# Performance work log

Hardware: AMD Instinct MI355X
Metric: run time of the kernel (lower is better)

The kernel has to match this reference:

```python
import jax, jax.numpy as jnp
import numpy as np

HID = 768
NH = 12
HD = HID // NH
EPS = 1e-12


def _layernorm(x, g, b):
    m = x.mean(-1, keepdims=True)
    v = ((x - m) ** 2).mean(-1, keepdims=True)
    return (x - m) / jnp.sqrt(v + EPS) * g + b


def _mha_block(x, mask, Wq, bq, Wk, bk, Wv, bv, Wo, bo, ln_g, ln_b):
    # x: [B,S,H]; mask broadcastable to [B,NH,S,S] (additive)
    B, S, _ = x.shape
    split = lambda t: t.reshape(B, S, NH, HD).transpose(0, 2, 1, 3)  # [B,NH,S,HD]
    q = split(x @ Wq + bq)
    k = split(x @ Wk + bk)
    v = split(x @ Wv + bv)
    scores = jnp.einsum('bhqd,bhkd->bhqk', q, k) / np.float32(np.sqrt(HD)) + mask
    probs = jax.nn.softmax(scores, axis=-1)
    ctx = jnp.einsum('bhqk,bhkd->bhqd', probs, v)
    ctx = ctx.transpose(0, 2, 1, 3).reshape(B, S, HID)
    # BertSelfOutput: dense + residual + LayerNorm
    return _layernorm(ctx @ Wo + bo + x, ln_g, ln_b)


def setup_inputs() -> dict:
    key = jax.random.key(0)
    ks = jax.random.split(key, 32)
    B, S = 32, 512
    scale = 0.02
    W = lambda i, di, do: jax.random.normal(ks[i], (di, do), jnp.float32) * scale
    inp = {
        'hidden_states': jax.random.normal(ks[0], (B, S, HID), jnp.float32),
        'attention_mask': jnp.zeros((B, 1, 1, S), jnp.float32),
        # token-level attention params
        'Wq': W(1, HID, HID), 'bq': jnp.zeros((HID,), jnp.float32),
        'Wk': W(2, HID, HID), 'bk': jnp.zeros((HID,), jnp.float32),
        'Wv': W(3, HID, HID), 'bv': jnp.zeros((HID,), jnp.float32),
        'Wao': W(4, HID, HID), 'bao': jnp.zeros((HID,), jnp.float32),
        'ln1_g': jnp.ones((HID,), jnp.float32), 'ln1_b': jnp.zeros((HID,), jnp.float32),
        # dialog (CLS-level) attention params
        'dWq': W(5, HID, HID), 'dbq': jnp.zeros((HID,), jnp.float32),
        'dWk': W(6, HID, HID), 'dbk': jnp.zeros((HID,), jnp.float32),
        'dWv': W(7, HID, HID), 'dbv': jnp.zeros((HID,), jnp.float32),
        'dWo': W(8, HID, HID), 'dbo': jnp.zeros((HID,), jnp.float32),
        'dln_g': jnp.ones((HID,), jnp.float32), 'dln_b': jnp.zeros((HID,), jnp.float32),
        # FFN params
        'Wi': W(9, HID, 4 * HID), 'bi': jnp.zeros((4 * HID,), jnp.float32),
        'Wo2': W(10, 4 * HID, HID), 'bo2': jnp.zeros((HID,), jnp.float32),
        'ln2_g': jnp.ones((HID,), jnp.float32), 'ln2_b': jnp.zeros((HID,), jnp.float32),
        'turns': 8,
    }
    return inp


def reference(hidden_states, attention_mask,
              Wq, bq, Wk, bk, Wv, bv, Wao, bao, ln1_g, ln1_b,
              dWq, dbq, dWk, dbk, dWv, dbv, dWo, dbo, dln_g, dln_b,
              Wi, bi, Wo2, bo2, ln2_g, ln2_b, turns):
    # 1) token-level self-attention + SelfOutput
    x = _mha_block(hidden_states, attention_mask,
                   Wq, bq, Wk, bk, Wv, bv, Wao, bao, ln1_g, ln1_b)
    # 2) hierarchical dialog attention over per-turn CLS tokens
    bs = x.shape[0] // turns
    cls = x[:, 0].reshape(bs, turns, HID)
    pos = jnp.arange(turns)
    # faithful to source: (j >= i) -> -10000 (masks diagonal and future)
    cmask = (pos[None, :] >= pos[:, None]).astype(x.dtype) * (-10000.0)
    cmask = cmask[None, None, :, :]  # broadcast to [bs, NH, turns, turns]
    cls = _mha_block(cls, cmask, dWq, dbq, dWk, dbk, dWv, dbv, dWo, dbo, dln_g, dln_b)
    x = x.at[:, 0].set(cls.reshape(-1, HID))
    # 3) FFN: intermediate (gelu) + output dense + residual + LayerNorm
    inter = jax.nn.gelu(x @ Wi + bi, approximate=False)
    out = _layernorm(inter @ Wo2 + bo2 + x, ln2_g, ln2_b)
    return out
```

## Files before the change

### kernel.cpp

```cpp
#include <hip/hip_runtime.h>
#include <hip/hip_bf16.h>
#include <math.h>

using bf16 = __hip_bfloat16;
typedef __attribute__((ext_vector_type(8))) __bf16 bf16x8;
typedef __attribute__((ext_vector_type(4))) float f32x4;

__device__ __forceinline__ float b2f(bf16 x){ return __bfloat162float(x); }
__device__ __forceinline__ bf16  f2b(float x){ return __float2bfloat16(x); }
__device__ __forceinline__ float ldf(const float* p, size_t i){ return p[i]; }
__device__ __forceinline__ float ldf(const bf16*  p, size_t i){ return b2f(p[i]); }
__device__ __forceinline__ void stf(float* p, size_t i, float v){ p[i] = v; }
__device__ __forceinline__ void stf(bf16*  p, size_t i, float v){ p[i] = f2b(v); }

__device__ __forceinline__ float gelu_f(float v){
  float u = v*(0.7978845608f + 0.0356774081f*v*v);
  float e = __expf(2.f*u);
  float t = 1.f - 2.f/(e+1.f);
  return 0.5f*v*(1.f+t);
}

typedef const __attribute__((address_space(1))) unsigned int* gas_u32p;
typedef __attribute__((address_space(3))) unsigned int* las_u32p;
__device__ __forceinline__ void gl_lds16(const bf16* g, bf16* l){
  __builtin_amdgcn_global_load_lds((gas_u32p)(const void*)g, (las_u32p)(void*)l, 16, 0, 0);
}

#define MFMA16 __builtin_amdgcn_mfma_f32_16x16x32_bf16

#define LGKM(N) do { \
  asm volatile("s_waitcnt lgkmcnt(" #N ")" ::: "memory"); \
  __builtin_amdgcn_sched_barrier(0); \
} while(0)

#define NHEAD 12
#define HDIM  64
#define HID   768
#define SEQ   512
#define BATCH 32
#define ROWS  (BATCH*SEQ)
#define QKVW  2304
#define QCH   128
#define NCHUNK (SEQ/QCH)
#define FT    128

template<int EPI, typename TR>
__global__ __launch_bounds__(512,2)
void gemm8p(const bf16* __restrict__ A, int lda,
            const bf16* __restrict__ Bt, int ldb,
            bf16* __restrict__ C, int ldc, int K,
            const float* __restrict__ bias,
            const TR* __restrict__ res, int ldres)
{
  __shared__ __align__(16) bf16 tileLds[4][256*64];

  const int tid  = threadIdx.x;
  const int wave = tid>>6, lane = tid&63;
  const int r = lane&15, qd = lane>>4;
  const int wr = wave>>2, wc = wave&3;
  const int m0 = blockIdx.y*256, n0 = blockIdx.x*256;
  const int NTK = K>>6;
  const int wbase = wave*512;

  const int sr = tid>>3, sp = tid&7;
  const bf16* pA = A  + (size_t)(m0+sr)*lda + ((sp^(sr&7))<<3);
  const bf16* pB = Bt + (size_t)(n0+sr)*ldb + ((sp^(sr&7))<<3);

  auto stage = [&](int H){
    const int u = H>>2, idx = H&3, bufi = u&1;
    const size_t kof = (size_t)u*64;
    if (idx==0){
      gl_lds16(pA + kof,                    tileLds[bufi*2] + wbase);
      gl_lds16(pA + kof + (size_t)64*lda,   tileLds[bufi*2] + wbase + 4096);
    } else if (idx==3){
      gl_lds16(pA + kof + (size_t)128*lda,  tileLds[bufi*2] + 8192 + wbase);
      gl_lds16(pA + kof + (size_t)192*lda,  tileLds[bufi*2] + 8192 + wbase + 4096);
    } else {
      const int h = idx-1;
      gl_lds16(pB + kof + (size_t)(h*128)*ldb,
               tileLds[bufi*2+1] + h*8192 + wbase);
      gl_lds16(pB + kof + (size_t)(h*128+64)*ldb,
               tileLds[bufi*2+1] + h*8192 + wbase + 4096);
    }
  };

  auto rdA = [&](const bf16* base, int mi, int ks)->bf16x8{
    const int row = mi*32 + wr*16 + r;
    return *(const bf16x8*)(base + row*64 + ((((ks<<2)|qd) ^ (r&7))<<3));
  };
  auto rdB = [&](const bf16* base, int nj, int ks)->bf16x8{
    const int row = nj*64 + wc*16 + r;
    return *(const bf16x8*)(base + row*64 + ((((ks<<2)|qd) ^ (r&7))<<3));
  };

  #pragma unroll
  for (int H=0; H<7; ++H) stage(H);
  asm volatile("s_waitcnt vmcnt(6)" ::: "memory");
  __builtin_amdgcn_s_barrier();

  f32x4 acc[8][4] = {};

  for (int t=0; t<NTK; ++t){
    const bf16* a = tileLds[(t&1)*2];
    const bf16* b = tileLds[(t&1)*2+1];
    const int Hb = 4*t + 6;
    const int Hmax = 4*NTK;
    bf16x8 af[4][2], bn0[2][2], bn1[2][2];

    af[0][0]=rdA(a,0,0); af[0][1]=rdA(a,0,1);
    af[1][0]=rdA(a,1,0); af[1][1]=rdA(a,1,1);
    bn0[0][0]=rdB(b,0,0); bn0[0][1]=rdB(b,0,1);
    bn0[1][0]=rdB(b,1,0); bn0[1][1]=rdB(b,1,1);
    __builtin_amdgcn_sched_barrier(0);
    af[2][0]=rdA(a,2,0); af[2][1]=rdA(a,2,1);
    af[3][0]=rdA(a,3,0); af[3][1]=rdA(a,3,1);
    if (Hb+1 < Hmax) stage(Hb+1);
    LGKM(4);
    __builtin_amdgcn_s_setprio(1);
    #pragma unroll
    for (int mi=0;mi<2;mi++)
      #pragma unroll
      for (int nj=0;nj<2;nj++){
        acc[mi][nj] = MFMA16(af[mi][0], bn0[nj][0], acc[mi][nj],0,0,0);
        acc[mi][nj] = MFMA16(af[mi][1], bn0[nj][1], acc[mi][nj],0,0,0);
      }
    LGKM(0);
    #pragma unroll
    for (int mi=2;mi<4;mi++)
      #pragma unroll
      for (int nj=0;nj<2;nj++){
        acc[mi][nj] = MFMA16(af[mi][0], bn0[nj][0], acc[mi][nj],0,0,0);
        acc[mi][nj] = MFMA16(af[mi][1], bn0[nj][1], acc[mi][nj],0,0,0);
      }
    __builtin_amdgcn_s_setprio(0);
    __builtin_amdgcn_s_barrier();

    bn1[0][0]=rdB(b,2,0); bn1[0][1]=rdB(b,2,1);
    __builtin_amdgcn_sched_barrier(0);
    bn1[1][0]=rdB(b,3,0); bn1[1][1]=rdB(b,3,1);
    if (Hb+2 < Hmax) stage(Hb+2);
    LGKM(2);
    __builtin_amdgcn_s_setprio(1);
    #pragma unroll
    for (int mi=0;mi<4;mi++){
      acc[mi][2] = MFMA16(af[mi][0], bn1[0][0], acc[mi][2],0,0,0);
      acc[mi][2] = MFMA16(af[mi][1], bn1[0][1], acc[mi][2],0,0,0);
    }
    LGKM(0);
    #pragma unroll
    for (int mi=0;mi<4;mi++){
      acc[mi][3] = MFMA16(af[mi][0], bn1[1][0], acc[mi][3],0,0,0);
      acc[mi][3] = MFMA16(af[mi][1], bn1[1][1], acc[mi][3],0,0,0);
    }
    __builtin_amdgcn_s_setprio(0);
    __builtin_amdgcn_s_barrier();

    af[0][0]=rdA(a,4,0); af[0][1]=rdA(a,4,1);
    af[1][0]=rdA(a,5,0); af[1][1]=rdA(a,5,1);
    __builtin_amdgcn_sched_barrier(0);
    af[2][0]=rdA(a,6,0); af[2][1]=rdA(a,6,1);
    af[3][0]=rdA(a,7,0); af[3][1]=rdA(a,7,1);
    if (Hb+3 < Hmax) stage(Hb+3);
    LGKM(4);
    __builtin_amdgcn_s_setprio(1);
    #pragma unroll
    for (int mi=0;mi<2;mi++)
      #pragma unroll
      for (int nj=0;nj<2;nj++){
        acc[4+mi][2+nj] = MFMA16(af[mi][0], bn1[nj][0], acc[4+mi][2+nj],0,0,0);
        acc[4+mi][2+nj] = MFMA16(af[mi][1], bn1[nj][1], acc[4+mi][2+nj],0,0,0);
      }
    LGKM(0);
    #pragma unroll
    for (int mi=2;mi<4;mi++)
      #pragma unroll
      for (int nj=0;nj<2;nj++){
        acc[4+mi][2+nj] = MFMA16(af[mi][0], bn1[nj][0], acc[4+mi][2+nj],0,0,0);
        acc[4+mi][2+nj] = MFMA16(af[mi][1], bn1[nj][1], acc[4+mi][2+nj],0,0,0);
      }
    __builtin_amdgcn_s_setprio(0);
    __builtin_amdgcn_s_barrier();

    if (Hb+4 < Hmax) stage(Hb+4);
    __builtin_amdgcn_s_setprio(1);
    #pragma unroll
    for (int mi=0;mi<4;mi++)
      #pragma unroll
      for (int nj=0;nj<2;nj++){
        acc[4+mi][nj] = MFMA16(af[mi][0], bn0[nj][0], acc[4+mi][nj],0,0,0);
        acc[4+mi][nj] = MFMA16(af[mi][1], bn0[nj][1], acc[4+mi][nj],0,0,0);
      }
    __builtin_amdgcn_s_setprio(0);
    if (t < NTK-2) { asm volatile("s_waitcnt vmcnt(6)" ::: "memory"); }
    else           { asm volatile("s_waitcnt vmcnt(0)" ::: "memory"); }
    __builtin_amdgcn_s_barrier();
  }

  float bs[4];
  #pragma unroll
  for (int nj=0;nj<4;nj++)
    bs[nj] = bias ? bias[n0 + nj*64 + wc*16 + r] : 0.f;
  #pragma unroll
  for (int mi=0;mi<8;mi++){
    #pragma unroll
    for (int nj=0;nj<4;nj++){
      #pragma unroll
      for (int i=0;i<4;i++){
        const int mm = m0 + mi*32 + wr*16 + qd*4 + i;
        const int nn = n0 + nj*64 + wc*16 + r;
        float v = acc[mi][nj][i] + bs[nj];
        if (EPI==1) v = gelu_f(v);
        if (EPI==2) v += ldf(res, (size_t)mm*ldres + nn);
        C[(size_t)mm*ldc + nn] = f2b(v);
      }
    }
  }
}

__global__ __launch_bounds__(256)
void flash_attn(const bf16* __restrict__ qkv, const bf16* __restrict__ vtb,
                const float* __restrict__ mask, bf16* __restrict__ ctx)
{
  const int qc = blockIdx.x;
  const int z  = blockIdx.y;
  const int b  = z / NHEAD, h = z - b*NHEAD;
  const int q0 = qc*QCH;

  __shared__ __align__(16) bf16 Qs[QCH*64];
  __shared__ __align__(16) bf16 Ks[FT*64];
  __shared__ __align__(16) bf16 Vts[64*FT];
  __shared__ float smask[FT];
  bf16* Ps = Ks;

  const int tid = threadIdx.x;
  const int wave = tid>>6, lane = tid&63;
  const int r = lane&15, qd = lane>>4;
  const int wr = wave;

  const bf16* Qg = qkv + ((size_t)(b*SEQ + q0))*QKVW + h*HDIM;
  const bf16* Kg = qkv + ((size_t)b*SEQ)*QKVW + 768 + h*HDIM;
  const bf16* Vg = vtb + (size_t)z*HDIM*SEQ;

  for (int c0=0;c0<1024;c0+=256){
    int c = c0+tid, row = c>>3, pos = c&7;
    gl_lds16(Qg + (size_t)row*QKVW + ((pos^(row&7))*8),
             Qs + (size_t)(c0 + wave*64)*8);
  }

  f32x4 accO[2][4] = {};
  float mrun[2][4], lrun[2][4];
  #pragma unroll
  for (int a=0;a<2;a++)
    #pragma unroll
    for (int i2=0;i2<4;i2++){ mrun[a][i2]=-1e30f; lrun[a][i2]=0.f; }

  for (int k0=0; k0<SEQ; k0+=FT){
    __syncthreads();
    for (int c0=0;c0<1024;c0+=256){
      int c = c0+tid, row = c>>3, pos = c&7;
      gl_lds16(Kg + (size_t)(k0+row)*QKVW + ((pos^(row&7))*8),
               Ks + (size_t)(c0 + wave*64)*8);
    }
    for (int c0=0;c0<1024;c0+=256){
      int c = c0+tid, row = c>>4, pos = c&15;
      gl_lds16(Vg + (size_t)row*SEQ + k0 + ((pos^(row&7))*8),
               Vts + (size_t)(c0 + wave*64)*8);
    }
    if (tid < FT) smask[tid] = mask[(size_t)b*SEQ + k0 + tid];
    __syncthreads();

    f32x4 accS[2][8] = {};
    #pragma unroll
    for (int ks=0; ks<2; ks++){
      bf16x8 af[2], bfv[8];
      #pragma unroll
      for (int mi=0;mi<2;mi++){
        int row = wr*32 + mi*16 + r;
        int jr = ks*4 + qd;
        af[mi] = *(const bf16x8*)(Qs + row*64 + ((jr^(row&7))*8));
      }
      #pragma unroll
      for (int ni=0;ni<8;ni++){
        int row = ni*16 + r;
        int jr = ks*4 + qd;
        bfv[ni] = *(const bf16x8*)(Ks + row*64 + ((jr^(row&7))*8));
      }
      #pragma unroll
      for (int mi=0;mi<2;mi++)
        #pragma unroll
        for (int ni=0;ni<8;ni++)
          accS[mi][ni] = MFMA16(af[mi], bfv[ni], accS[mi][ni], 0,0,0);
    }

    #pragma unroll
    for (int mi=0;mi<2;mi++){
      #pragma unroll
      for (int i=0;i<4;i++){
        float mx = -1e30f;
        #pragma unroll
        for (int ni=0;ni<8;ni++){
          float v = accS[mi][ni][i]*0.125f + smask[ni*16+r];
          accS[mi][ni][i] = v;
          mx = fmaxf(mx, v);
        }
        #pragma unroll
        for (int off=1; off<16; off<<=1) mx = fmaxf(mx, __shfl_xor(mx, off));
        float mnew = fmaxf(mrun[mi][i], mx);
        float alpha = __expf(mrun[mi][i] - mnew);
        mrun[mi][i] = mnew;
        float ssum = 0.f;
        #pragma unroll
        for (int ni=0;ni<8;ni++){
          float p = __expf(accS[mi][ni][i] - mnew);
          accS[mi][ni][i] = p;
          ssum += p;
        }
        #pragma unroll
        for (int off=1; off<16; off<<=1) ssum += __shfl_xor(ssum, off);
        lrun[mi][i] = lrun[mi][i]*alpha + ssum;
        #pragma unroll
        for (int ni=0;ni<4;ni++) accO[mi][ni][i] *= alpha;
      }
    }

    #pragma unroll
    for (int half=0; half<2; half++){
      __syncthreads();
      #pragma unroll
      for (int mi=0;mi<2;mi++){
        #pragma unroll
        for (int i=0;i<4;i++){
          int row = wr*32 + mi*16 + qd*4 + i;
          #pragma unroll
          for (int nj=0;nj<4;nj++){
            int colL = nj*16 + r;
            int chunk = colL>>3;
            Ps[row*64 + ((chunk^(row&7))*8) + (colL&7)] = f2b(accS[mi][half*4+nj][i]);
          }
        }
      }
      __syncthreads();
      #pragma unroll
      for (int ks=0; ks<2; ks++){
        bf16x8 af[2], bfv[4];
        #pragma unroll
        for (int mi=0;mi<2;mi++){
          int row = wr*32 + mi*16 + r;
          int jr = ks*4 + qd;
          af[mi] = *(const bf16x8*)(Ps + row*64 + ((jr^(row&7))*8));
        }
        #pragma unroll
        for (int ni=0;ni<4;ni++){
          int row = ni*16 + r;
          int jrv = half*8 + ks*4 + qd;
          bfv[ni] = *(const bf16x8*)(Vts + row*FT + ((jrv^(row&7))*8));
        }
        #pragma unroll
        for (int mi=0;mi<2;mi++)
          #pragma unroll
          for (int ni=0;ni<4;ni++)
            accO[mi][ni] = MFMA16(af[mi], bfv[ni], accO[mi][ni], 0,0,0);
      }
    }
  }

  bf16* Cg = ctx + ((size_t)(b*SEQ + q0))*HID + h*HDIM;
  #pragma unroll
  for (int mi=0;mi<2;mi++)
    #pragma unroll
    for (int i=0;i<4;i++){
      int row = wr*32 + mi*16 + qd*4 + i;
      float invl = 1.0f/lrun[mi][i];
      #pragma unroll
      for (int ni=0;ni<4;ni++)
        Cg[(size_t)row*HID + ni*16 + r] = f2b(accO[mi][ni][i]*invl);
    }
}

__global__ void transpose_cast(const float* __restrict__ in, bf16* __restrict__ out,
                               int R, int C)
{
  __shared__ float tile[32][33];
  int bc = blockIdx.x*32, br = blockIdx.y*32;
  int tx = threadIdx.x, ty = threadIdx.y;
  #pragma unroll
  for (int i=ty;i<32;i+=8)
    tile[i][tx] = in[(size_t)(br+i)*C + bc+tx];
  __syncthreads();
  #pragma unroll
  for (int i=ty;i<32;i+=8)
    out[(size_t)(bc+i)*R + br+tx] = f2b(tile[tx][i]);
}

__global__ void transpose_cast4(const float* __restrict__ w0, const float* __restrict__ w1,
                                const float* __restrict__ w2, const float* __restrict__ w3,
                                bf16* __restrict__ out)
{
  const float* in = blockIdx.z==0?w0 : blockIdx.z==1?w1 : blockIdx.z==2?w2 : w3;
  bf16* o = out + (size_t)blockIdx.z*768*768;
  __shared__ float tile[32][33];
  int bc = blockIdx.x*32, br = blockIdx.y*32;
  int tx = threadIdx.x, ty = threadIdx.y;
  #pragma unroll
  for (int i=ty;i<32;i+=8)
    tile[i][tx] = in[(size_t)(br+i)*768 + bc+tx];
  __syncthreads();
  #pragma unroll
  for (int i=ty;i<32;i+=8)
    o[(size_t)(bc+i)*768 + br+tx] = f2b(tile[tx][i]);
}

__global__ __launch_bounds__(256)
void castX(const float* __restrict__ in, bf16* __restrict__ out)
{
  int i = blockIdx.x*256 + threadIdx.x;
  float4 f = ((const float4*)in)[i];
  union{ unsigned long long u; __bf16 h[4]; } pk;
  pk.h[0]=(__bf16)f.x; pk.h[1]=(__bf16)f.y; pk.h[2]=(__bf16)f.z; pk.h[3]=(__bf16)f.w;
  ((unsigned long long*)out)[i] = pk.u;
}

__global__ void concat_bias(const float* __restrict__ a, const float* __restrict__ b,
                            const float* __restrict__ c, float* __restrict__ o)
{
  int i = blockIdx.x*256 + threadIdx.x;
  if (i < 768) o[i] = a[i];
  else if (i < 1536) o[i] = b[i-768];
  else if (i < 2304) o[i] = c[i-1536];
}

__global__ void vtrans(const bf16* __restrict__ v, bf16* __restrict__ vt)
{
  int z = blockIdx.z; int b = z/NHEAD, h = z - b*NHEAD;
  int d0 = blockIdx.x*32, s0 = blockIdx.y*32;
  __shared__ bf16 t[32][33];
  int tx = threadIdx.x, ty = threadIdx.y;
  #pragma unroll
  for (int i=ty;i<32;i+=8)
    t[i][tx] = v[(size_t)(b*SEQ + s0+i)*QKVW + h*HDIM + d0+tx];
  __syncthreads();
  #pragma unroll
  for (int i=ty;i<32;i+=8)
    vt[(size_t)z*HDIM*SEQ + (size_t)(d0+i)*SEQ + s0+tx] = t[tx][i];
}

template<typename TO>
__global__ __launch_bounds__(256)
void ln768(const bf16* __restrict__ y, const float* __restrict__ g,
           const float* __restrict__ be, TO* __restrict__ dst)
{
  size_t row = blockIdx.x;
  const bf16* yr = y + row*HID;
  int t = threadIdx.x;
  float x0 = b2f(yr[t]), x1 = b2f(yr[t+256]), x2 = b2f(yr[t+512]);
  float s = x0+x1+x2, q = x0*x0+x1*x1+x2*x2;
  #pragma unroll
  for (int off=32; off; off>>=1){ s += __shfl_xor(s, off); q += __shfl_xor(q, off); }
  __shared__ float rs[4], rq[4];
  int wv = t>>6;
  if ((t&63)==0){ rs[wv]=s; rq[wv]=q; }
  __syncthreads();
  s = rs[0]+rs[1]+rs[2]+rs[3];
  q = rq[0]+rq[1]+rq[2]+rq[3];
  float mean = s*(1.0f/HID);
  float var  = q*(1.0f/HID) - mean*mean;
  float inv  = rsqrtf(var + 1e-12f);
  TO* dr = dst + row*HID;
  stf(dr, t,     (x0-mean)*inv*g[t    ] + be[t    ]);
  stf(dr, t+256, (x1-mean)*inv*g[t+256] + be[t+256]);
  stf(dr, t+512, (x2-mean)*inv*g[t+512] + be[t+512]);
}

__global__ __launch_bounds__(256)
void cls_proj(const bf16* __restrict__ x2,
              const float* __restrict__ Wq, const float* __restrict__ bq,
              const float* __restrict__ Wk, const float* __restrict__ bk,
              const float* __restrict__ Wv, const float* __restrict__ bv,
              bf16* __restrict__ oq, bf16* __restrict__ ok, bf16* __restrict__ ov)
{
  int mat = blockIdx.x, row = blockIdx.y;
  const float* W  = mat==0 ? Wq : (mat==1 ? Wk : Wv);
  const float* bi = mat==0 ? bq : (mat==1 ? bk : bv);
  bf16* out       = mat==0 ? oq : (mat==1 ? ok : ov);
  __shared__ float a[HID];
  const bf16* xr = x2 + (size_t)row*SEQ*HID;
  for (int i=threadIdx.x;i<HID;i+=256) a[i] = b2f(xr[i]);
  __syncthreads();
  for (int c0=0;c0<HID;c0+=256){
    int col = c0 + threadIdx.x;
    float acc = 0.f;
    for (int k=0;k<HID;k++) acc += a[k]*W[(size_t)k*HID + col];
    out[(size_t)row*HID + col] = f2b(acc + bi[col]);
  }
}

__global__ __launch_bounds__(64)
void cls_attn(const bf16* __restrict__ q, const bf16* __restrict__ k,
              const bf16* __restrict__ v, bf16* __restrict__ ctx)
{
  int z = blockIdx.x; int bb = z/NHEAD, h = z - bb*NHEAD;
  __shared__ float P[8][8];
  int t = threadIdx.x;
  int qi = t>>3, ki = t&7;
  float s = 0.f;
  for (int d=0; d<HDIM; d++)
    s += b2f(q[(size_t)(bb*8+qi)*HID + h*HDIM + d]) *
         b2f(k[(size_t)(bb*8+ki)*HID + h*HDIM + d]);
  s = s*0.125f + (ki >= qi ? -10000.0f : 0.0f);
  float m = s;
  #pragma unroll
  for (int off=4; off; off>>=1) m = fmaxf(m, __shfl_xor(m, off, 8));
  float e = __expf(s - m);
  float sum = e;
  #pragma unroll
  for (int off=4; off; off>>=1) sum += __shfl_xor(sum, off, 8);
  P[qi][ki] = e/sum;
  __syncthreads();
  for (int q2=0; q2<8; q2++){
    float acc = 0.f;
    #pragma unroll
    for (int k2=0; k2<8; k2++)
      acc += P[q2][k2] * b2f(v[(size_t)(bb*8+k2)*HID + h*HDIM + t]);
    ctx[(size_t)(bb*8+q2)*HID + h*HDIM + t] = f2b(acc);
  }
}

__global__ __launch_bounds__(256)
void cls_out(const bf16* __restrict__ ctx, const float* __restrict__ Wo,
             const float* __restrict__ bo, const float* __restrict__ g,
             const float* __restrict__ be, bf16* __restrict__ x2)
{
  int row = blockIdx.x;
  __shared__ float a[HID];
  __shared__ float yrow[HID];
  const bf16* cr = ctx + (size_t)row*HID;
  bf16* xr = x2 + (size_t)row*SEQ*HID;
  for (int i=threadIdx.x;i<HID;i+=256) a[i] = b2f(cr[i]);
  __syncthreads();
  for (int c0=0;c0<HID;c0+=256){
    int col = c0 + threadIdx.x;
    float acc = 0.f;
    for (int k=0;k<HID;k++) acc += a[k]*Wo[(size_t)k*HID + col];
    yrow[col] = acc + bo[col] + b2f(xr[col]);
  }
  __syncthreads();
  int t = threadIdx.x;
  float x0 = yrow[t], x1 = yrow[t+256], x2v = yrow[t+512];
  float s = x0+x1+x2v, qq = x0*x0+x1*x1+x2v*x2v;
  #pragma unroll
  for (int off=32; off; off>>=1){ s += __shfl_xor(s, off); qq += __shfl_xor(qq, off); }
  __shared__ float rs[4], rq[4];
  int wv = t>>6;
  if ((t&63)==0){ rs[wv]=s; rq[wv]=qq; }
  __syncthreads();
  s = rs[0]+rs[1]+rs[2]+rs[3];
  qq = rq[0]+rq[1]+rq[2]+rq[3];
  float mean = s*(1.0f/HID);
  float var  = qq*(1.0f/HID) - mean*mean;
  float inv  = rsqrtf(var + 1e-12f);
  xr[t    ] = f2b((x0 -mean)*inv*g[t    ] + be[t    ]);
  xr[t+256] = f2b((x1 -mean)*inv*g[t+256] + be[t+256]);
  xr[t+512] = f2b((x2v-mean)*inv*g[t+512] + be[t+512]);
}

extern "C" void kernel_launch(void* const* d_in, const int* in_sizes, int n_in,
                              void* d_out, int out_size, void* d_ws, size_t ws_size,
                              hipStream_t stream)
{
  const float* X    = (const float*)d_in[0];
  const float* AM   = (const float*)d_in[1];
  const float* Wq   = (const float*)d_in[2];  const float* bq  = (const float*)d_in[3];
  const float* Wk   = (const float*)d_in[4];  const float* bk  = (const float*)d_in[5];
  const float* Wv   = (const float*)d_in[6];  const float* bv  = (const float*)d_in[7];
  const float* Wao  = (const float*)d_in[8];  const float* bao = (const float*)d_in[9];
  const float* ln1g = (const float*)d_in[10]; const float* ln1b= (const float*)d_in[11];
  const float* dWq  = (const float*)d_in[12]; const float* dbq = (const float*)d_in[13];
  const float* dWk  = (const float*)d_in[14]; const float* dbk = (const float*)d_in[15];
  const float* dWv  = (const float*)d_in[16]; const float* dbv = (const float*)d_in[17];
  const float* dWo  = (const float*)d_in[18]; const float* dbo = (const float*)d_in[19];
  const float* dlng = (const float*)d_in[20]; const float* dlnb= (const float*)d_in[21];
  const float* Wi   = (const float*)d_in[22]; const float* bi  = (const float*)d_in[23];
  const float* Wo2  = (const float*)d_in[24]; const float* bo2 = (const float*)d_in[25];
  const float* ln2g = (const float*)d_in[26]; const float* ln2b= (const float*)d_in[27];
  float* OUT = (float*)d_out;

  char* wp = (char*)d_ws;
  auto alloc = [&](size_t elems)->bf16*{
    bf16* p = (bf16*)wp;
    wp += ((elems*sizeof(bf16) + 255)/256)*256;
    return p;
  };
  bf16* wtq  = alloc(768*768);
  bf16* wtk  = alloc(768*768);
  bf16* wtv  = alloc(768*768);
  bf16* wtao = alloc(768*768);
  bf16* wti  = alloc((size_t)768*3072);
  bf16* wto2 = alloc((size_t)3072*768);
  float* bqkv = (float*)alloc(2304*2);
  bf16* qkv  = alloc((size_t)ROWS*QKVW);
  bf16* vtb  = alloc((size_t)ROWS*HID);
  bf16* inter = qkv;
  bf16* scb  = alloc((size_t)ROWS*HID);
  bf16* yb   = scb;
  bf16* x2   = scb;
  bf16* ctxb = alloc((size_t)ROWS*HID);
  bf16* xb   = ctxb;
  bf16* clsq = alloc(32*HID);
  bf16* clsk = alloc(32*HID);
  bf16* clsv = alloc(32*HID);
  bf16* clsc = alloc(32*HID);
  (void)wtk; (void)wtv;

  dim3 T32(32,8);
  transpose_cast4<<<dim3(24,24,4), T32, 0, stream>>>(Wq, Wk, Wv, Wao, wtq);
  transpose_cast<<<dim3(96,24), T32, 0, stream>>>(Wi,  wti, 768, 3072);
  transpose_cast<<<dim3(24,96), T32, 0, stream>>>(Wo2, wto2,3072, 768);
  concat_bias<<<9,256,0,stream>>>(bq, bk, bv, bqkv);
  castX<<<ROWS*HID/4/256,256,0,stream>>>(X, xb);

  gemm8p<0,float><<<dim3(9,64),512,0,stream>>>(
      xb,768,  wtq,768,  qkv,QKVW, 768, bqkv, (const float*)nullptr, 0);

  vtrans<<<dim3(2,16,BATCH*NHEAD), T32, 0, stream>>>(qkv + 1536, vtb);

  flash_attn<<<dim3(NCHUNK, BATCH*NHEAD),256,0,stream>>>(qkv, vtb, AM, ctxb);

  gemm8p<2,float><<<dim3(3,64),512,0,stream>>>(
      ctxb,768,  wtao,768,  yb,768, 768, bao, X, 768);
  ln768<bf16><<<ROWS,256,0,stream>>>(yb, ln1g, ln1b, x2);

  cls_proj<<<dim3(3,32),256,0,stream>>>(x2, dWq,dbq, dWk,dbk, dWv,dbv,
                                        clsq, clsk, clsv);
  cls_attn<<<48,64,0,stream>>>(clsq, clsk, clsv, clsc);
  cls_out<<<32,256,0,stream>>>(clsc, dWo, dbo, dlng, dlnb, x2);

  gemm8p<1,float><<<dim3(12,64),512,0,stream>>>(
      x2,768,  wti,768,  inter,3072, 768, bi, (const float*)nullptr, 0);
  gemm8p<2,bf16><<<dim3(3,64),512,0,stream>>>(
      inter,3072,  wto2,3072,  yb,768, 3072, bo2, x2, 768);
  ln768<float><<<ROWS,256,0,stream>>>(yb, ln2g, ln2b, OUT);
}
```

Before: 825.8 us.

## Prefetch next K/V tiles during compute and keep Q in registers in flash attention

Restructures the flash-attention loop so the next K tile is loaded right after the QK^T MFMAs and the next V tile right after the PV MFMAs. This overlaps global-to-LDS traffic with softmax and matmul work. Q fragments are now loaded once straight into registers, and P gets its own LDS buffer so the two per-half barriers can be dropped. The softmax switches to exp2 with pre-scaled logits and reads mask values into registers instead of through shared memory. The cost is more register pressure, and correctness now depends on each wave touching only its own P rows.

After: 829.0 us. No clear change (+0.4%).

```diff
diff --git a/kernel.cpp b/kernel.cpp
--- a/kernel.cpp
+++ b/kernel.cpp
@@ -43,6 +43,7 @@
 #define QCH   128
 #define NCHUNK (SEQ/QCH)
 #define FT    128
+#define LOG2E 1.44269504f
 
 template<int EPI, typename TR>
 __global__ __launch_bounds__(512,2)
@@ -226,11 +227,9 @@
   const int b  = z / NHEAD, h = z - b*NHEAD;
   const int q0 = qc*QCH;
 
-  __shared__ __align__(16) bf16 Qs[QCH*64];
   __shared__ __align__(16) bf16 Ks[FT*64];
   __shared__ __align__(16) bf16 Vts[64*FT];
-  __shared__ float smask[FT];
-  bf16* Ps = Ks;
+  __shared__ __align__(16) bf16 Ps[QCH*64];
 
   const int tid = threadIdx.x;
   const int wave = tid>>6, lane = tid&63;
@@ -241,44 +240,53 @@
   const bf16* Kg = qkv + ((size_t)b*SEQ)*QKVW + 768 + h*HDIM;
   const bf16* Vg = vtb + (size_t)z*HDIM*SEQ;
 
-  for (int c0=0;c0<1024;c0+=256){
-    int c = c0+tid, row = c>>3, pos = c&7;
-    gl_lds16(Qg + (size_t)row*QKVW + ((pos^(row&7))*8),
-             Qs + (size_t)(c0 + wave*64)*8);
-  }
-
-  f32x4 accO[2][4] = {};
-  float mrun[2][4], lrun[2][4];
-  #pragma unroll
-  for (int a=0;a<2;a++)
-    #pragma unroll
-    for (int i2=0;i2<4;i2++){ mrun[a][i2]=-1e30f; lrun[a][i2]=0.f; }
-
-  for (int k0=0; k0<SEQ; k0+=FT){
-    __syncthreads();
+  auto stageK = [&](int k0){
+    #pragma unroll
     for (int c0=0;c0<1024;c0+=256){
       int c = c0+tid, row = c>>3, pos = c&7;
       gl_lds16(Kg + (size_t)(k0+row)*QKVW + ((pos^(row&7))*8),
                Ks + (size_t)(c0 + wave*64)*8);
     }
+  };
+  auto stageV = [&](int k0){
+    #pragma unroll
     for (int c0=0;c0<1024;c0+=256){
       int c = c0+tid, row = c>>4, pos = c&15;
       gl_lds16(Vg + (size_t)row*SEQ + k0 + ((pos^(row&7))*8),
                Vts + (size_t)(c0 + wave*64)*8);
     }
-    if (tid < FT) smask[tid] = mask[(size_t)b*SEQ + k0 + tid];
+  };
+
+  stageK(0);
+  stageV(0);
+  bf16x8 qf[2][2];
+  #pragma unroll
+  for (int mi=0;mi<2;mi++)
+    #pragma unroll
+    for (int ks=0;ks<2;ks++)
+      qf[mi][ks] = *(const bf16x8*)(Qg + (size_t)(wr*32+mi*16+r)*QKVW + (ks*4+qd)*8);
+
+  f32x4 accO[2][4] = {};
+  float mrun[2][4], lrun[2][4];
+  #pragma unroll
+  for (int a=0;a<2;a++)
+    #pragma unroll
+    for (int i2=0;i2<4;i2++){ mrun[a][i2]=-1e30f; lrun[a][i2]=0.f; }
+
+  const float SC2 = 0.125f*LOG2E;
+
+  for (int k0=0; k0<SEQ; k0+=FT){
     __syncthreads();
 
+    float mk[8];
+    #pragma unroll
+    for (int ni=0;ni<8;ni++)
+      mk[ni] = mask[(size_t)b*SEQ + k0 + ni*16 + r] * LOG2E;
+
     f32x4 accS[2][8] = {};
     #pragma unroll
     for (int ks=0; ks<2; ks++){
-      bf16x8 af[2], bfv[8];
-      #pragma unroll
-      for (int mi=0;mi<2;mi++){
-        int row = wr*32 + mi*16 + r;
-        int jr = ks*4 + qd;
-        af[mi] = *(const bf16x8*)(Qs + row*64 + ((jr^(row&7))*8));
-      }
+      bf16x8 bfv[8];
       #pragma unroll
       for (int ni=0;ni<8;ni++){
         int row = ni*16 + r;
@@ -289,8 +297,11 @@
       for (int mi=0;mi<2;mi++)
         #pragma unroll
         for (int ni=0;ni<8;ni++)
-          accS[mi][ni] = MFMA16(af[mi], bfv[ni], accS[mi][ni], 0,0,0);
-    }
+          accS[mi][ni] = MFMA16(qf[mi][ks], bfv[ni], accS[mi][ni], 0,0,0);
+    }
+
+    __syncthreads();
+    if (k0+FT < SEQ) stageK(k0+FT);
 
     #pragma unroll
     for (int mi=0;mi<2;mi++){
@@ -299,19 +310,19 @@
         float mx = -1e30f;
         #pragma unroll
         for (int ni=0;ni<8;ni++){
-          float v = accS[mi][ni][i]*0.125f + smask[ni*16+r];
+          float v = accS[mi][ni][i]*SC2 + mk[ni];
           accS[mi][ni][i] = v;
           mx = fmaxf(mx, v);
         }
         #pragma unroll
         for (int off=1; off<16; off<<=1) mx = fmaxf(mx, __shfl_xor(mx, off));
         float mnew = fmaxf(mrun[mi][i], mx);
-        float alpha = __expf(mrun[mi][i] - mnew);
+        float alpha = exp2f(mrun[mi][i] - mnew);
         mrun[mi][i] = mnew;
         float ssum = 0.f;
         #pragma unroll
         for (int ni=0;ni<8;ni++){
-          float p = __expf(accS[mi][ni][i] - mnew);
+          float p = exp2f(accS[mi][ni][i] - mnew);
           accS[mi][ni][i] = p;
           ssum += p;
         }
@@ -325,7 +336,6 @@
 
     #pragma unroll
     for (int half=0; half<2; half++){
-      __syncthreads();
       #pragma unroll
       for (int mi=0;mi<2;mi++){
         #pragma unroll
@@ -339,7 +349,6 @@
           }
         }
       }
-      __syncthreads();
       #pragma unroll
       for (int ks=0; ks<2; ks++){
         bf16x8 af[2], bfv[4];
@@ -362,6 +371,9 @@
             accO[mi][ni] = MFMA16(af[mi], bfv[ni], accO[mi][ni], 0,0,0);
       }
     }
+
+    __syncthreads();
+    if (k0+FT < SEQ) stageV(k0+FT);
   }
 
   bf16* Cg = ctx + ((size_t)(b*SEQ + q0))*HID + h*HDIM;
```
